# Kernel tuning notes

Hardware: AMD Instinct MI355X
Metric: run time of the kernel (lower is better)

Reference implementation:

```python
import jax, jax.numpy as jnp
import numpy as np

F = 26          # field_size
D = 16          # embed_dim
B = 16384       # batch
VOCABS = [1000] * F
OFFSETS = np.concatenate([[0], np.cumsum(VOCABS)[:-1]]).astype(np.int32)
IU, JU = np.triu_indices(F, k=1)   # 325 pairs (i<j)
P = IU.shape[0]
BN_EPS = 1e-3   # Keras BatchNormalization default epsilon


def setup_inputs() -> dict:
    key = jax.random.key(0)
    ks = jax.random.split(key, 8)
    s = 0.05  # keras 'random_normal' initializer stddev
    return {
        "x": jax.random.randint(ks[0], (B, F), 0, 1000, dtype=jnp.int32),
        "emb_table": jax.random.normal(ks[1], (sum(VOCABS) + 1, D), jnp.float32) * s,
        "se_w1": jax.random.normal(ks[2], (F, F // 2), jnp.float32) * s,
        "se_w2": jax.random.normal(ks[3], (F // 2, F), jnp.float32) * s,
        "bl_w": jax.random.normal(ks[4], (P, D, D), jnp.float32) * s,
        "w1": jax.random.normal(ks[5], (F * (F - 1) * D, 64), jnp.float32) * s,
        "b1": jnp.zeros((64,), jnp.float32),
        "g1": jnp.ones((64,), jnp.float32),
        "be1": jnp.zeros((64,), jnp.float32),
        "m1": jnp.zeros((64,), jnp.float32),
        "v1": jnp.ones((64,), jnp.float32),
        "w2": jax.random.normal(ks[6], (64, 32), jnp.float32) * s,
        "b2": jnp.zeros((32,), jnp.float32),
        "g2": jnp.ones((32,), jnp.float32),
        "be2": jnp.zeros((32,), jnp.float32),
        "m2": jnp.zeros((32,), jnp.float32),
        "v2": jnp.ones((32,), jnp.float32),
        "w3": jax.random.normal(ks[7], (32, 1), jnp.float32) * s,
        "b3": jnp.zeros((1,), jnp.float32),
    }


def _bilinear(v, bl_w):
    # v: [B, F, D]; shared W stack over the 325 ordered pairs (i<j)
    # tmp[p] = (v_i @ W_p) * v_j  -> [B, P, D]
    return jnp.einsum('bpd,pde->bpe', v[:, IU], bl_w) * v[:, JU]


def _bn(h, g, b, m, v):
    return g * (h - m) * jax.lax.rsqrt(v + BN_EPS) + b


def reference(x, emb_table, se_w1, se_w2, bl_w,
              w1, b1, g1, be1, m1, v1,
              w2, b2, g2, be2, m2, v2,
              w3, b3):
    ids = x + jnp.asarray(OFFSETS)
    e = emb_table[ids]                         # [B, F, D]
    # SE layer: mean-pool over embed dim, two ReLU dense layers, rescale
    z = e.mean(axis=-1)                        # [B, F]
    A = jax.nn.relu(jax.nn.relu(z @ se_w1) @ se_w2)
    se = e * A[..., None]                      # [B, F, D]
    # Bilinear interaction (same weights for both calls)
    p = _bilinear(e, bl_w).reshape(e.shape[0], -1)     # [B, P*D]
    se_p = _bilinear(se, bl_w).reshape(e.shape[0], -1)
    h = jnp.concatenate([p, se_p], axis=-1)    # [B, F*(F-1)*D]
    # MLP with inference-mode BatchNorm; dropout=0 is a no-op
    h = jax.nn.relu(_bn(h @ w1 + b1, g1, be1, m1, v1))
    h = jax.nn.relu(_bn(h @ w2 + b2, g2, be2, m2, v2))
    return jax.nn.sigmoid(h @ w3 + b3)         # [B, 1]
```

## Files before the change

kernel.cpp:

```cpp
#include <hip/hip_runtime.h>
#include <cstdint>
#include <cstddef>


#define F_FIELDS 26
#define P_PAIRS 325
#define PAD_PAIRS 336
#define BATCH 16384
#define BN_EPS 1e-3f

typedef short bf16x8 __attribute__((ext_vector_type(8)));
typedef float f32x4 __attribute__((ext_vector_type(4)));

struct PairTab { unsigned char iu[PAD_PAIRS]; unsigned char ju[PAD_PAIRS]; };
static constexpr PairTab make_pairs() {
    PairTab t{};
    int p = 0;
    for (int a = 0; a < F_FIELDS; ++a)
        for (int b = a + 1; b < F_FIELDS; ++b) { t.iu[p] = (unsigned char)a; t.ju[p] = (unsigned char)b; ++p; }
    for (; p < PAD_PAIRS; ++p) { t.iu[p] = 0; t.ju[p] = 0; }
    return t;
}
__constant__ PairTab PT = make_pairs();

__device__ __forceinline__ unsigned short bf16u(float v) {
    unsigned u = __float_as_uint(v);
    unsigned r = (u + 0x7fffu + ((u >> 16) & 1u)) >> 16;
    return (unsigned short)r;
}
__device__ __forceinline__ unsigned pk_bf16(float lo, float hi) {
    return (unsigned)bf16u(lo) | ((unsigned)bf16u(hi) << 16);
}
__device__ __forceinline__ float bflo(unsigned d) { return __uint_as_float(d << 16); }
__device__ __forceinline__ float bfhi(unsigned d) { return __uint_as_float(d & 0xffff0000u); }
__device__ __forceinline__ unsigned pk_trunc(float u, float cu) {
    return __builtin_amdgcn_perm(__float_as_uint(cu), __float_as_uint(u), 0x07060302u);
}

__global__ __launch_bounds__(256) void k_wprep(const float* __restrict__ w1,
        const float* __restrict__ blw, unsigned short* __restrict__ w1catL,
        unsigned short* __restrict__ wcatL) {
    const int p = blockIdx.x;
    const int tid = threadIdx.x;
    if (p >= P_PAIRS) {
        int4 z = make_int4(0, 0, 0, 0);
        *(int4*)(w1catL + (size_t)p * 2048 + tid * 8) = z;
        if (tid < 64) *(int4*)(wcatL + (size_t)p * 512 + tid * 8) = z;
        return;
    }
    __shared__ float wu[1024], wv[1024], wb[256];
    ((float4*)wu)[tid] = ((const float4*)(w1 + (size_t)p * 1024))[tid];
    ((float4*)wv)[tid] = ((const float4*)(w1 + 332800 + (size_t)p * 1024))[tid];
    if (tid < 64) ((float4*)wb)[tid] = ((const float4*)(blw + (size_t)p * 256))[tid];
    __syncthreads();
    {
        int nt = tid >> 6, lane = tid & 63, ln = lane & 15, q = lane >> 4;
        int o = nt * 16 + ln;
        unsigned short outv[8];
        #pragma unroll
        for (int j = 0; j < 8; ++j) {
            int k = q * 8 + j, d = k >> 1, su = k & 1;
            outv[j] = bf16u(su ? wv[d * 64 + o] : wu[d * 64 + o]);
        }
        *(int4*)(w1catL + (size_t)p * 2048 + tid * 8) = *(const int4*)outv;
    }
    if (tid < 64) {
        int ln = tid & 15, q = tid >> 4;
        unsigned short outv[8];
        #pragma unroll
        for (int j = 0; j < 8; ++j) {
            int din = q * 8 + j;
            outv[j] = (din < 16) ? bf16u(wb[din * 16 + ln]) : (unsigned short)0;
        }
        *(int4*)(wcatL + (size_t)p * 512 + tid * 8) = *(const int4*)outv;
    }
}

__global__ __launch_bounds__(512, 4) void k_main(const int* __restrict__ x,
        const float* __restrict__ emb, const float* __restrict__ sw1,
        const float* __restrict__ sw2, const unsigned short* __restrict__ w1catL,
        const unsigned short* __restrict__ wcatL, unsigned* __restrict__ ybuf) {
    __shared__ __align__(16) unsigned short eS[32 * 424];
    __shared__ float aS[F_FIELDS * 32];
    __shared__ float z_s[32][F_FIELDS];
    __shared__ float sw1_s[F_FIELDS * 13];
    __shared__ float sw2_s[13 * F_FIELDS];
    const int tid = threadIdx.x;
    const int b0 = blockIdx.x * 32;

    for (int i = tid; i < F_FIELDS * 13; i += 512) { sw1_s[i] = sw1[i]; sw2_s[i] = sw2[i]; }
    for (int idx = tid; idx < 32 * F_FIELDS; idx += 512) {
        int r = idx / F_FIELDS, f = idx - r * F_FIELDS;
        int id = x[(b0 + r) * F_FIELDS + f] + f * 1000;
        const float4* src = (const float4*)(emb + (size_t)id * 16);
        float4 v0 = src[0], v1 = src[1], v2 = src[2], v3 = src[3];
        int4 o0, o1;
        o0.x = (int)pk_bf16(v0.x, v0.y); o0.y = (int)pk_bf16(v0.z, v0.w);
        o0.z = (int)pk_bf16(v1.x, v1.y); o0.w = (int)pk_bf16(v1.z, v1.w);
        o1.x = (int)pk_bf16(v2.x, v2.y); o1.y = (int)pk_bf16(v2.z, v2.w);
        o1.z = (int)pk_bf16(v3.x, v3.y); o1.w = (int)pk_bf16(v3.z, v3.w);
        *(int4*)(eS + r * 424 + f * 16) = o0;
        *(int4*)(eS + r * 424 + f * 16 + 8) = o1;
        float s = v0.x + v0.y + v0.z + v0.w + v1.x + v1.y + v1.z + v1.w
                + v2.x + v2.y + v2.z + v2.w + v3.x + v3.y + v3.z + v3.w;
        z_s[r][f] = s * (1.0f / 16.0f);
    }
    __syncthreads();
    if (tid < 32) {
        float s1[13];
        #pragma unroll
        for (int o = 0; o < 13; ++o) {
            float acc0 = 0.f;
            #pragma unroll
            for (int f = 0; f < F_FIELDS; ++f) acc0 = fmaf(z_s[tid][f], sw1_s[f * 13 + o], acc0);
            s1[o] = fmaxf(acc0, 0.0f);
        }
        #pragma unroll
        for (int f = 0; f < F_FIELDS; ++f) {
            float acc0 = 0.f;
            #pragma unroll
            for (int o = 0; o < 13; ++o) acc0 = fmaf(s1[o], sw2_s[o * F_FIELDS + f], acc0);
            aS[f * 32 + tid] = fmaxf(acc0, 0.0f);
        }
    }
    __syncthreads();

    const int w    = tid >> 6;
    const int lane = tid & 63;
    const int ln   = lane & 15;
    const int q    = lane >> 4;
    const int p0 = w * 42, p1 = p0 + 42;

    f32x4 acc[2][4];
    #pragma unroll
    for (int a = 0; a < 2; ++a)
        #pragma unroll
        for (int b = 0; b < 4; ++b) acc[a][b] = (f32x4){0.f, 0.f, 0.f, 0.f};
    const f32x4 zero4 = {0.f, 0.f, 0.f, 0.f};

    int iu_c = PT.iu[p0];
    bf16x8 eiB[2];
    float ai[2];
    #pragma unroll
    for (int mt = 0; mt < 2; ++mt) {
        eiB[mt] = __builtin_bit_cast(bf16x8,
            *(const int4*)(eS + (mt * 16 + ln) * 424 + iu_c * 16 + (q & 1) * 8));
        ai[mt] = aS[iu_c * 32 + mt * 16 + ln];
    }
    bf16x8 wa_c = __builtin_bit_cast(bf16x8, *(const int4*)(wcatL + (size_t)p0 * 512 + lane * 8));
    bf16x8 wb_c[4];
    #pragma unroll
    for (int nt = 0; nt < 4; ++nt)
        wb_c[nt] = __builtin_bit_cast(bf16x8, *(const int4*)(w1catL + (size_t)p0 * 2048 + nt * 512 + lane * 8));

    #pragma unroll 2
    for (int p = p0; p < p1; ++p) {
        const int pn = (p + 1 < p1) ? (p + 1) : p;
        bf16x8 wa_n = __builtin_bit_cast(bf16x8, *(const int4*)(wcatL + (size_t)pn * 512 + lane * 8));
        bf16x8 wb_n[4];
        #pragma unroll
        for (int nt = 0; nt < 4; ++nt)
            wb_n[nt] = __builtin_bit_cast(bf16x8, *(const int4*)(w1catL + (size_t)pn * 2048 + nt * 512 + lane * 8));

        const int ju = PT.ju[p];
        uint2 ejv[2];
        float cv[2];
        #pragma unroll
        for (int mt = 0; mt < 2; ++mt) {
            ejv[mt] = *(const uint2*)(eS + (mt * 16 + ln) * 424 + ju * 16 + q * 4);
            cv[mt]  = ai[mt] * aS[ju * 32 + mt * 16 + ln];
        }
        #pragma unroll
        for (int mt = 0; mt < 2; ++mt) {
            f32x4 t = __builtin_amdgcn_mfma_f32_16x16x32_bf16(wa_c, eiB[mt], zero4, 0, 0, 0);
            float e0 = bflo(ejv[mt].x), e1 = bfhi(ejv[mt].x);
            float e2 = bflo(ejv[mt].y), e3 = bfhi(ejv[mt].y);
            float c  = cv[mt];
            float u0 = t[0] * e0, u1 = t[1] * e1, u2 = t[2] * e2, u3 = t[3] * e3;
            int4 af;
            af.x = (int)pk_trunc(u0, c * u0);
            af.y = (int)pk_trunc(u1, c * u1);
            af.z = (int)pk_trunc(u2, c * u2);
            af.w = (int)pk_trunc(u3, c * u3);
            bf16x8 A = __builtin_bit_cast(bf16x8, af);
            #pragma unroll
            for (int nt = 0; nt < 4; ++nt)
                acc[mt][nt] = __builtin_amdgcn_mfma_f32_16x16x32_bf16(A, wb_c[nt], acc[mt][nt], 0, 0, 0);
        }
        const int iu_n = PT.iu[pn];
        if (iu_n != iu_c) {
            iu_c = iu_n;
            #pragma unroll
            for (int mt = 0; mt < 2; ++mt) {
                eiB[mt] = __builtin_bit_cast(bf16x8,
                    *(const int4*)(eS + (mt * 16 + ln) * 424 + iu_c * 16 + (q & 1) * 8));
                ai[mt] = aS[iu_c * 32 + mt * 16 + ln];
            }
        }
        wa_c = wa_n;
        #pragma unroll
        for (int nt = 0; nt < 4; ++nt) wb_c[nt] = wb_n[nt];
    }

    const size_t ub = ((size_t)w * 512 + blockIdx.x) * 1024;
    #pragma unroll
    for (int mt = 0; mt < 2; ++mt)
        #pragma unroll
        for (int nh = 0; nh < 2; ++nh) {
            int nt0 = nh * 2, nt1 = nh * 2 + 1;
            int4 v;
            v.x = (int)pk_bf16(acc[mt][nt0][0], acc[mt][nt0][1]);
            v.y = (int)pk_bf16(acc[mt][nt0][2], acc[mt][nt0][3]);
            v.z = (int)pk_bf16(acc[mt][nt1][0], acc[mt][nt1][1]);
            v.w = (int)pk_bf16(acc[mt][nt1][2], acc[mt][nt1][3]);
            *(int4*)(ybuf + ub + (mt * 2 + nh) * 256 + lane * 4) = v;
        }
}

__global__ __launch_bounds__(256) void k_epi(
        const unsigned* __restrict__ ybuf,
        const float* __restrict__ b1, const float* __restrict__ g1,
        const float* __restrict__ be1, const float* __restrict__ m1,
        const float* __restrict__ v1,
        const float* __restrict__ w2, const float* __restrict__ b2,
        const float* __restrict__ g2, const float* __restrict__ be2,
        const float* __restrict__ m2, const float* __restrict__ v2,
        const float* __restrict__ w3, const float* __restrict__ b3,
        float* __restrict__ out) {
    __shared__ __align__(16) float h1s[64 * 64];
    __shared__ float h2s[64 * 36];
    const int tid = threadIdx.x;
    const int blk = blockIdx.x;
    const int b0 = blk * 64;
    const int lane = tid & 63, ln = lane & 15, q = lane >> 4;
    const int nh = (tid >> 6) & 1, mt = tid >> 7;
    const int c0 = nh * 32 + ln, c1 = nh * 32 + 16 + ln;

    const float sc0 = g1[c0] * rsqrtf(v1[c0] + BN_EPS);
    const float of0 = be1[c0] + sc0 * (b1[c0] - m1[c0]);
    const float sc1 = g1[c1] * rsqrtf(v1[c1] + BN_EPS);
    const float of1 = be1[c1] + sc1 * (b1[c1] - m1[c1]);

    #pragma unroll
    for (int mg2 = 0; mg2 < 2; ++mg2) {
        const int mg = blk * 2 + mg2;
        float s8[8];
        #pragma unroll
        for (int i = 0; i < 8; ++i) s8[i] = 0.f;
        const size_t ub = (size_t)mg * 1024 + (size_t)tid * 4;
        #pragma unroll
        for (int w = 0; w < 8; ++w) {
            int4 v = *(const int4*)(ybuf + (size_t)w * 512 * 1024 + ub);
            s8[0] += bflo((unsigned)v.x); s8[1] += bfhi((unsigned)v.x);
            s8[2] += bflo((unsigned)v.y); s8[3] += bfhi((unsigned)v.y);
            s8[4] += bflo((unsigned)v.z); s8[5] += bfhi((unsigned)v.z);
            s8[6] += bflo((unsigned)v.w); s8[7] += bfhi((unsigned)v.w);
        }
        const int row0 = mg2 * 32 + mt * 16 + q * 4;
        #pragma unroll
        for (int r = 0; r < 4; ++r) {
            h1s[(row0 + r) * 64 + c0] = fmaxf(s8[r] * sc0 + of0, 0.f);
            h1s[(row0 + r) * 64 + c1] = fmaxf(s8[4 + r] * sc1 + of1, 0.f);
        }
    }
    __syncthreads();

    const int r2 = tid >> 2;
    const int og2 = (tid & 3) << 3;
    float a2[8];
    #pragma unroll
    for (int qq = 0; qq < 8; ++qq) a2[qq] = 0.f;
    #pragma unroll 8
    for (int k = 0; k < 64; ++k) {
        float hk = h1s[r2 * 64 + k];
        float4 wa = *(const float4*)(w2 + k * 32 + og2);
        float4 wb = *(const float4*)(w2 + k * 32 + og2 + 4);
        a2[0] = fmaf(hk, wa.x, a2[0]); a2[1] = fmaf(hk, wa.y, a2[1]);
        a2[2] = fmaf(hk, wa.z, a2[2]); a2[3] = fmaf(hk, wa.w, a2[3]);
        a2[4] = fmaf(hk, wb.x, a2[4]); a2[5] = fmaf(hk, wb.y, a2[5]);
        a2[6] = fmaf(hk, wb.z, a2[6]); a2[7] = fmaf(hk, wb.w, a2[7]);
    }
    #pragma unroll
    for (int qq = 0; qq < 8; ++qq) {
        int o = og2 + qq;
        float val = g2[o] * (a2[qq] + b2[o] - m2[o]) * rsqrtf(v2[o] + BN_EPS) + be2[o];
        h2s[r2 * 36 + o] = fmaxf(val, 0.f);
    }
    __syncthreads();
    if (tid < 64) {
        float sacc = b3[0];
        #pragma unroll
        for (int k = 0; k < 32; ++k) sacc = fmaf(h2s[tid * 36 + k], w3[k], sacc);
        out[b0 + tid] = 1.0f / (1.0f + expf(-sacc));
    }
}

extern "C" void kernel_launch(void* const* d_in, const int* in_sizes, int n_in,
                              void* d_out, int out_size, void* d_ws, size_t ws_size,
                              hipStream_t stream) {
    const int*   x   = (const int*)d_in[0];
    const float* emb = (const float*)d_in[1];
    const float* sw1 = (const float*)d_in[2];
    const float* sw2 = (const float*)d_in[3];
    const float* blw = (const float*)d_in[4];
    const float* w1  = (const float*)d_in[5];
    const float* b1  = (const float*)d_in[6];
    const float* g1  = (const float*)d_in[7];
    const float* be1 = (const float*)d_in[8];
    const float* m1  = (const float*)d_in[9];
    const float* v1  = (const float*)d_in[10];
    const float* w2  = (const float*)d_in[11];
    const float* b2  = (const float*)d_in[12];
    const float* g2  = (const float*)d_in[13];
    const float* be2 = (const float*)d_in[14];
    const float* m2  = (const float*)d_in[15];
    const float* v2  = (const float*)d_in[16];
    const float* w3  = (const float*)d_in[17];
    const float* b3  = (const float*)d_in[18];
    float* out = (float*)d_out;

    char* ws = (char*)d_ws;
    unsigned short* w1catL = (unsigned short*)ws;
    unsigned short* wcatL  = (unsigned short*)(ws + 1376256);
    unsigned*       ybuf   = (unsigned*)(ws + 1720320);

    hipLaunchKernelGGL(k_wprep, dim3(PAD_PAIRS), dim3(256), 0, stream, w1, blw, w1catL, wcatL);
    hipLaunchKernelGGL(k_main,  dim3(512), dim3(512), 0, stream,
                       x, emb, sw1, sw2, w1catL, wcatL, ybuf);
    hipLaunchKernelGGL(k_epi,   dim3(256), dim3(256), 0, stream, ybuf,
                       b1, g1, be1, m1, v1, w2, b2, g2, be2, m2, v2, w3, b3, out);
}
```

Measured before the change: 150.5 us.

## Fuse MLP epilogue into main kernel and software-pipeline the bilinear MFMA

The epilogue kernel is folded into the main kernel. Per-wave partial layer-1 outputs now go to shared memory, which is aliased with the embedding tile through a union, and each block reduces them and runs the BN/ReLU MLP and sigmoid for its own 32 rows. This drops the ybuf global round trip and one kernel launch. Separately, the first bilinear MFMA for the next pair is issued one iteration ahead, so its latency overlaps the current pair's accumulation MFMAs. The cost is more registers and extra barriers, and the small epilogue now runs with 512 threads over only 32 rows.

```diff
diff --git a/kernel.cpp b/kernel.cpp
--- a/kernel.cpp
+++ b/kernel.cpp
@@ -76,33 +76,54 @@
     }
 }
 
+union __align__(16) SMem {
+    struct {
+        unsigned short eS[32 * 424];
+        float aS[F_FIELDS * 32];
+    } a;
+    struct {
+        unsigned ysh[8 * 4 * 64 * 4];
+        float h1s[32 * 65];
+        float h2s[32 * 36];
+    } b;
+};
+
 __global__ __launch_bounds__(512, 4) void k_main(const int* __restrict__ x,
         const float* __restrict__ emb, const float* __restrict__ sw1,
         const float* __restrict__ sw2, const unsigned short* __restrict__ w1catL,
-        const unsigned short* __restrict__ wcatL, unsigned* __restrict__ ybuf) {
-    __shared__ __align__(16) unsigned short eS[32 * 424];
-    __shared__ float aS[F_FIELDS * 32];
+        const unsigned short* __restrict__ wcatL,
+        const float* __restrict__ b1, const float* __restrict__ g1,
+        const float* __restrict__ be1, const float* __restrict__ m1,
+        const float* __restrict__ v1,
+        const float* __restrict__ w2, const float* __restrict__ b2,
+        const float* __restrict__ g2, const float* __restrict__ be2,
+        const float* __restrict__ m2, const float* __restrict__ v2,
+        const float* __restrict__ w3, const float* __restrict__ b3,
+        float* __restrict__ out) {
+    __shared__ SMem sm;
     __shared__ float z_s[32][F_FIELDS];
     __shared__ float sw1_s[F_FIELDS * 13];
     __shared__ float sw2_s[13 * F_FIELDS];
     const int tid = threadIdx.x;
     const int b0 = blockIdx.x * 32;
+    unsigned short* eS = sm.a.eS;
+    float* aS = sm.a.aS;
 
     for (int i = tid; i < F_FIELDS * 13; i += 512) { sw1_s[i] = sw1[i]; sw2_s[i] = sw2[i]; }
     for (int idx = tid; idx < 32 * F_FIELDS; idx += 512) {
         int r = idx / F_FIELDS, f = idx - r * F_FIELDS;
         int id = x[(b0 + r) * F_FIELDS + f] + f * 1000;
         const float4* src = (const float4*)(emb + (size_t)id * 16);
-        float4 v0 = src[0], v1 = src[1], v2 = src[2], v3 = src[3];
+        float4 v0 = src[0], v1l = src[1], v2l = src[2], v3l = src[3];
         int4 o0, o1;
-        o0.x = (int)pk_bf16(v0.x, v0.y); o0.y = (int)pk_bf16(v0.z, v0.w);
-        o0.z = (int)pk_bf16(v1.x, v1.y); o0.w = (int)pk_bf16(v1.z, v1.w);
-        o1.x = (int)pk_bf16(v2.x, v2.y); o1.y = (int)pk_bf16(v2.z, v2.w);
-        o1.z = (int)pk_bf16(v3.x, v3.y); o1.w = (int)pk_bf16(v3.z, v3.w);
+        o0.x = (int)pk_bf16(v0.x, v0.y);  o0.y = (int)pk_bf16(v0.z, v0.w);
+        o0.z = (int)pk_bf16(v1l.x, v1l.y); o0.w = (int)pk_bf16(v1l.z, v1l.w);
+        o1.x = (int)pk_bf16(v2l.x, v2l.y); o1.y = (int)pk_bf16(v2l.z, v2l.w);
+        o1.z = (int)pk_bf16(v3l.x, v3l.y); o1.w = (int)pk_bf16(v3l.z, v3l.w);
         *(int4*)(eS + r * 424 + f * 16) = o0;
         *(int4*)(eS + r * 424 + f * 16 + 8) = o1;
-        float s = v0.x + v0.y + v0.z + v0.w + v1.x + v1.y + v1.z + v1.w
-                + v2.x + v2.y + v2.z + v2.w + v3.x + v3.y + v3.z + v3.w;
+        float s = v0.x + v0.y + v0.z + v0.w + v1l.x + v1l.y + v1l.z + v1l.w
+                + v2l.x + v2l.y + v2l.z + v2l.w + v3l.x + v3l.y + v3l.z + v3l.w;
         z_s[r][f] = s * (1.0f / 16.0f);
     }
     __syncthreads();
@@ -152,6 +173,10 @@
     #pragma unroll
     for (int nt = 0; nt < 4; ++nt)
         wb_c[nt] = __builtin_bit_cast(bf16x8, *(const int4*)(w1catL + (size_t)p0 * 2048 + nt * 512 + lane * 8));
+    f32x4 tc[2];
+    #pragma unroll
+    for (int mt = 0; mt < 2; ++mt)
+        tc[mt] = __builtin_amdgcn_mfma_f32_16x16x32_bf16(wa_c, eiB[mt], zero4, 0, 0, 0);
 
     #pragma unroll 2
     for (int p = p0; p < p1; ++p) {
@@ -170,9 +195,24 @@
             ejv[mt] = *(const uint2*)(eS + (mt * 16 + ln) * 424 + ju * 16 + q * 4);
             cv[mt]  = ai[mt] * aS[ju * 32 + mt * 16 + ln];
         }
+        const int iu_n = PT.iu[pn];
+        if (iu_n != iu_c) {
+            iu_c = iu_n;
+            #pragma unroll
+            for (int mt = 0; mt < 2; ++mt) {
+                eiB[mt] = __builtin_bit_cast(bf16x8,
+                    *(const int4*)(eS + (mt * 16 + ln) * 424 + iu_c * 16 + (q & 1) * 8));
+                ai[mt] = aS[iu_c * 32 + mt * 16 + ln];
+            }
+        }
+        f32x4 tn[2];
+        #pragma unroll
+        for (int mt = 0; mt < 2; ++mt)
+            tn[mt] = __builtin_amdgcn_mfma_f32_16x16x32_bf16(wa_n, eiB[mt], zero4, 0, 0, 0);
+
         #pragma unroll
         for (int mt = 0; mt < 2; ++mt) {
-            f32x4 t = __builtin_amdgcn_mfma_f32_16x16x32_bf16(wa_c, eiB[mt], zero4, 0, 0, 0);
+            f32x4 t = tc[mt];
             float e0 = bflo(ejv[mt].x), e1 = bfhi(ejv[mt].x);
             float e2 = bflo(ejv[mt].y), e3 = bfhi(ejv[mt].y);
             float c  = cv[mt];
@@ -187,22 +227,16 @@
             for (int nt = 0; nt < 4; ++nt)
                 acc[mt][nt] = __builtin_amdgcn_mfma_f32_16x16x32_bf16(A, wb_c[nt], acc[mt][nt], 0, 0, 0);
         }
-        const int iu_n = PT.iu[pn];
-        if (iu_n != iu_c) {
-            iu_c = iu_n;
-            #pragma unroll
-            for (int mt = 0; mt < 2; ++mt) {
-                eiB[mt] = __builtin_bit_cast(bf16x8,
-                    *(const int4*)(eS + (mt * 16 + ln) * 424 + iu_c * 16 + (q & 1) * 8));
-                ai[mt] = aS[iu_c * 32 + mt * 16 + ln];
-            }
-        }
+        tc[0] = tn[0]; tc[1] = tn[1];
         wa_c = wa_n;
         #pragma unroll
         for (int nt = 0; nt < 4; ++nt) wb_c[nt] = wb_n[nt];
     }
 
-    const size_t ub = ((size_t)w * 512 + blockIdx.x) * 1024;
+    __syncthreads();
+    unsigned* ysh = sm.b.ysh;
+    float* h1s = sm.b.h1s;
+    float* h2s = sm.b.h2s;
     #pragma unroll
     for (int mt = 0; mt < 2; ++mt)
         #pragma unroll
@@ -213,81 +247,56 @@
             v.y = (int)pk_bf16(acc[mt][nt0][2], acc[mt][nt0][3]);
             v.z = (int)pk_bf16(acc[mt][nt1][0], acc[mt][nt1][1]);
             v.w = (int)pk_bf16(acc[mt][nt1][2], acc[mt][nt1][3]);
-            *(int4*)(ybuf + ub + (mt * 2 + nh) * 256 + lane * 4) = v;
-        }
-}
-
-__global__ __launch_bounds__(256) void k_epi(
-        const unsigned* __restrict__ ybuf,
-        const float* __restrict__ b1, const float* __restrict__ g1,
-        const float* __restrict__ be1, const float* __restrict__ m1,
-        const float* __restrict__ v1,
-        const float* __restrict__ w2, const float* __restrict__ b2,
-        const float* __restrict__ g2, const float* __restrict__ be2,
-        const float* __restrict__ m2, const float* __restrict__ v2,
-        const float* __restrict__ w3, const float* __restrict__ b3,
-        float* __restrict__ out) {
-    __shared__ __align__(16) float h1s[64 * 64];
-    __shared__ float h2s[64 * 36];
-    const int tid = threadIdx.x;
-    const int blk = blockIdx.x;
-    const int b0 = blk * 64;
-    const int lane = tid & 63, ln = lane & 15, q = lane >> 4;
-    const int nh = (tid >> 6) & 1, mt = tid >> 7;
-    const int c0 = nh * 32 + ln, c1 = nh * 32 + 16 + ln;
-
-    const float sc0 = g1[c0] * rsqrtf(v1[c0] + BN_EPS);
-    const float of0 = be1[c0] + sc0 * (b1[c0] - m1[c0]);
-    const float sc1 = g1[c1] * rsqrtf(v1[c1] + BN_EPS);
-    const float of1 = be1[c1] + sc1 * (b1[c1] - m1[c1]);
-
-    #pragma unroll
-    for (int mg2 = 0; mg2 < 2; ++mg2) {
-        const int mg = blk * 2 + mg2;
+            *(int4*)(ysh + ((w * 4 + mt * 2 + nh) * 64 + lane) * 4) = v;
+        }
+    __syncthreads();
+
+    if (tid < 256) {
+        const int s = tid >> 6, lane2 = tid & 63, ln2 = lane2 & 15, q2 = lane2 >> 4;
+        const int mt = s >> 1, nh = s & 1;
+        const int c0 = nh * 32 + ln2, c1 = c0 + 16;
+        const float sc0 = g1[c0] * rsqrtf(v1[c0] + BN_EPS);
+        const float of0 = be1[c0] + sc0 * (b1[c0] - m1[c0]);
+        const float sc1 = g1[c1] * rsqrtf(v1[c1] + BN_EPS);
+        const float of1 = be1[c1] + sc1 * (b1[c1] - m1[c1]);
         float s8[8];
         #pragma unroll
         for (int i = 0; i < 8; ++i) s8[i] = 0.f;
-        const size_t ub = (size_t)mg * 1024 + (size_t)tid * 4;
-        #pragma unroll
-        for (int w = 0; w < 8; ++w) {
-            int4 v = *(const int4*)(ybuf + (size_t)w * 512 * 1024 + ub);
+        #pragma unroll
+        for (int wv = 0; wv < 8; ++wv) {
+            int4 v = *(const int4*)(ysh + ((wv * 4 + s) * 64 + lane2) * 4);
             s8[0] += bflo((unsigned)v.x); s8[1] += bfhi((unsigned)v.x);
             s8[2] += bflo((unsigned)v.y); s8[3] += bfhi((unsigned)v.y);
             s8[4] += bflo((unsigned)v.z); s8[5] += bfhi((unsigned)v.z);
             s8[6] += bflo((unsigned)v.w); s8[7] += bfhi((unsigned)v.w);
         }
-        const int row0 = mg2 * 32 + mt * 16 + q * 4;
+        const int row0 = mt * 16 + q2 * 4;
         #pragma unroll
         for (int r = 0; r < 4; ++r) {
-            h1s[(row0 + r) * 64 + c0] = fmaxf(s8[r] * sc0 + of0, 0.f);
-            h1s[(row0 + r) * 64 + c1] = fmaxf(s8[4 + r] * sc1 + of1, 0.f);
-        }
-    }
-    __syncthreads();
-
-    const int r2 = tid >> 2;
-    const int og2 = (tid & 3) << 3;
-    float a2[8];
-    #pragma unroll
-    for (int qq = 0; qq < 8; ++qq) a2[qq] = 0.f;
-    #pragma unroll 8
-    for (int k = 0; k < 64; ++k) {
-        float hk = h1s[r2 * 64 + k];
-        float4 wa = *(const float4*)(w2 + k * 32 + og2);
-        float4 wb = *(const float4*)(w2 + k * 32 + og2 + 4);
-        a2[0] = fmaf(hk, wa.x, a2[0]); a2[1] = fmaf(hk, wa.y, a2[1]);
-        a2[2] = fmaf(hk, wa.z, a2[2]); a2[3] = fmaf(hk, wa.w, a2[3]);
-        a2[4] = fmaf(hk, wb.x, a2[4]); a2[5] = fmaf(hk, wb.y, a2[5]);
-        a2[6] = fmaf(hk, wb.z, a2[6]); a2[7] = fmaf(hk, wb.w, a2[7]);
-    }
-    #pragma unroll
-    for (int qq = 0; qq < 8; ++qq) {
-        int o = og2 + qq;
-        float val = g2[o] * (a2[qq] + b2[o] - m2[o]) * rsqrtf(v2[o] + BN_EPS) + be2[o];
-        h2s[r2 * 36 + o] = fmaxf(val, 0.f);
-    }
-    __syncthreads();
-    if (tid < 64) {
+            h1s[(row0 + r) * 65 + c0] = fmaxf(s8[r] * sc0 + of0, 0.f);
+            h1s[(row0 + r) * 65 + c1] = fmaxf(s8[4 + r] * sc1 + of1, 0.f);
+        }
+    }
+    __syncthreads();
+
+    {
+        const int row = tid >> 4, gg = tid & 15;
+        const int o0 = gg * 2, o1 = o0 + 1;
+        float a0 = 0.f, a1 = 0.f;
+        #pragma unroll 8
+        for (int k = 0; k < 64; ++k) {
+            float hk = h1s[row * 65 + k];
+            float2 wv = *(const float2*)(w2 + k * 32 + o0);
+            a0 = fmaf(hk, wv.x, a0);
+            a1 = fmaf(hk, wv.y, a1);
+        }
+        float val0 = g2[o0] * (a0 + b2[o0] - m2[o0]) * rsqrtf(v2[o0] + BN_EPS) + be2[o0];
+        float val1 = g2[o1] * (a1 + b2[o1] - m2[o1]) * rsqrtf(v2[o1] + BN_EPS) + be2[o1];
+        h2s[row * 36 + o0] = fmaxf(val0, 0.f);
+        h2s[row * 36 + o1] = fmaxf(val1, 0.f);
+    }
+    __syncthreads();
+    if (tid < 32) {
         float sacc = b3[0];
         #pragma unroll
         for (int k = 0; k < 32; ++k) sacc = fmaf(h2s[tid * 36 + k], w3[k], sacc);
@@ -322,11 +331,9 @@
     char* ws = (char*)d_ws;
     unsigned short* w1catL = (unsigned short*)ws;
     unsigned short* wcatL  = (unsigned short*)(ws + 1376256);
-    unsigned*       ybuf   = (unsigned*)(ws + 1720320);
 
     hipLaunchKernelGGL(k_wprep, dim3(PAD_PAIRS), dim3(256), 0, stream, w1, blw, w1catL, wcatL);
     hipLaunchKernelGGL(k_main,  dim3(512), dim3(512), 0, stream,
-                       x, emb, sw1, sw2, w1catL, wcatL, ybuf);
-    hipLaunchKernelGGL(k_epi,   dim3(256), dim3(256), 0, stream, ybuf,
+                       x, emb, sw1, sw2, w1catL, wcatL,
                        b1, g1, be1, m1, v1, w2, b2, g2, be2, m2, v2, w3, b3, out);
 }
```

New measurement: 144.7 us. 3.8% less time.
